# Kernel optimization log

Hardware: AMD Instinct MI355X
Metric: run time of the kernel (lower is better)

The kernel has to match this reference:

```python
import jax, jax.numpy as jnp
import numpy as np

HEADS = 16
DIM_HEAD = 64
LN_EPS = 1e-3  # keras LayerNormalization default


def setup_inputs() -> dict:
    key = jax.random.key(0)
    ks = jax.random.split(key, 4)
    B, N, D = 8, 512, 1024
    inner = HEADS * DIM_HEAD  # 1024
    return {
        "x": jax.random.normal(ks[0], (B, N, D), dtype=jnp.float32),
        "w_qkv": jax.random.normal(ks[1], (D, 3 * inner), dtype=jnp.float32) * (D ** -0.5),
        "reattn_w": jax.random.normal(ks[2], (HEADS, HEADS), dtype=jnp.float32),
        "ln_gamma": jnp.ones((HEADS,), dtype=jnp.float32),
        "ln_beta": jnp.zeros((HEADS,), dtype=jnp.float32),
        "w_out": jax.random.normal(ks[3], (inner, D), dtype=jnp.float32) * (inner ** -0.5),
        "b_out": jnp.zeros((D,), dtype=jnp.float32),
    }


def reference(x, w_qkv, reattn_w, ln_gamma, ln_beta, w_out, b_out):
    B, N, D = x.shape
    H, dh = HEADS, DIM_HEAD
    scale = dh ** -0.5

    qkv = x @ w_qkv  # [B, N, 3*H*dh]
    q, k, v = jnp.split(qkv, 3, axis=-1)
    # b n (h d) -> b h n d
    to_heads = lambda t: t.reshape(B, N, H, dh).transpose(0, 2, 1, 3)
    q, k, v = to_heads(q), to_heads(k), to_heads(v)

    dots = jnp.einsum("bhid,bhjd->bhij", q, k) * scale  # [B, H, N, N]
    attn = jax.nn.softmax(dots, axis=-1)

    # re-attention: mix across heads
    attn = jnp.einsum("bhij,hg->bgij", attn, reattn_w)

    # LayerNorm over the head axis (axis=1), keras default eps
    mean = jnp.mean(attn, axis=1, keepdims=True)
    var = jnp.var(attn, axis=1, keepdims=True)
    attn = (attn - mean) * jax.lax.rsqrt(var + LN_EPS)
    attn = attn * ln_gamma[None, :, None, None] + ln_beta[None, :, None, None]

    out = jnp.einsum("bhij,bhjd->bhid", attn, v)  # [B, H, N, dh]
    out = out.transpose(0, 2, 1, 3).reshape(B, N, H * dh)  # b h n d -> b n (h d)
    return out @ w_out + b_out
```

## Files before the change

### kernel.cpp

```cpp
#include <hip/hip_runtime.h>
#include <math.h>

#define BB 8
#define NN 512
#define DD 1024
#define HH 16
#define DH 64
#define INNER 1024
#define QKV3 3072

typedef __attribute__((ext_vector_type(8))) short short8;
typedef __attribute__((ext_vector_type(4))) float f32x4;

__device__ __forceinline__ float4 ld4(const float* p) { return *(const float4*)p; }

__device__ __forceinline__ unsigned short f2bf(float f) {
    unsigned u = __float_as_uint(f);
    return (unsigned short)((u + 0x7fffu + ((u >> 16) & 1u)) >> 16);
}
__device__ __forceinline__ float bf2f(unsigned short u) {
    return __uint_as_float(((unsigned)u) << 16);
}

__global__ void conv_bf16(const float* __restrict__ in, unsigned short* __restrict__ out) {
    size_t i = ((size_t)blockIdx.x * 256 + threadIdx.x) * 4;
    float4 v = ld4(in + i);
    ushort4 o;
    o.x = f2bf(v.x); o.y = f2bf(v.y); o.z = f2bf(v.z); o.w = f2bf(v.w);
    *(ushort4*)(out + i) = o;
}

__global__ void convT_bf16(const float* __restrict__ in, unsigned short* __restrict__ out,
                           int K, int N) {
    __shared__ float t[32][33];
    const int n0 = blockIdx.x * 32, k0 = blockIdx.y * 32;
    const int tx = threadIdx.x & 31, ty = threadIdx.x >> 5;
#pragma unroll
    for (int l = 0; l < 4; ++l)
        t[ty + 8 * l][tx] = in[(size_t)(k0 + ty + 8 * l) * N + n0 + tx];
    __syncthreads();
#pragma unroll
    for (int l = 0; l < 4; ++l)
        out[(size_t)(n0 + ty + 8 * l) * K + k0 + tx] = f2bf(t[tx][ty + 8 * l]);
}

__global__ __launch_bounds__(256) void gemm_bf16(
    const unsigned short* __restrict__ A, const unsigned short* __restrict__ Bt,
    float* __restrict__ C, const float* __restrict__ bias, int M, int N, int K) {
    __shared__ short As[128 * 32];
    __shared__ short Bs[128 * 32];
    const int tid = threadIdx.x;
    const int w = tid >> 6, l = tid & 63;
    const int bm = blockIdx.y * 128, bn = blockIdx.x * 128;
    const int wm = (w >> 1) * 64, wn = (w & 1) * 64;
    const int lrow = l & 15, lq = l >> 4;

    f32x4 acc[4][4];
#pragma unroll
    for (int i = 0; i < 4; ++i)
#pragma unroll
        for (int j = 0; j < 4; ++j) acc[i][j] = (f32x4){0.f, 0.f, 0.f, 0.f};

    for (int k0 = 0; k0 < K; k0 += 32) {
#pragma unroll
        for (int t = 0; t < 2; ++t) {
            const int q = w * 2 + t;
            const int li = q * 512 + l * 8;
            const int row = li >> 5, kc = li & 31;
            const unsigned short* ga = A + (size_t)(bm + row) * K + k0 + kc;
            __builtin_amdgcn_global_load_lds(
                (const __attribute__((address_space(1))) void*)ga,
                (__attribute__((address_space(3))) void*)(As + q * 512), 16, 0, 0);
            const unsigned short* gb = Bt + (size_t)(bn + row) * K + k0 + kc;
            __builtin_amdgcn_global_load_lds(
                (const __attribute__((address_space(1))) void*)gb,
                (__attribute__((address_space(3))) void*)(Bs + q * 512), 16, 0, 0);
        }
        __syncthreads();

        short8 a[4], b[4];
#pragma unroll
        for (int i = 0; i < 4; ++i)
            a[i] = *(const short8*)(As + (wm + i * 16 + lrow) * 32 + lq * 8);
#pragma unroll
        for (int j = 0; j < 4; ++j)
            b[j] = *(const short8*)(Bs + (wn + j * 16 + lrow) * 32 + lq * 8);
#pragma unroll
        for (int i = 0; i < 4; ++i)
#pragma unroll
            for (int j = 0; j < 4; ++j)
                acc[i][j] = __builtin_amdgcn_mfma_f32_16x16x32_bf16(a[i], b[j], acc[i][j], 0, 0, 0);
        __syncthreads();
    }

#pragma unroll
    for (int i = 0; i < 4; ++i)
#pragma unroll
        for (int j = 0; j < 4; ++j) {
            const int col = bn + wn + j * 16 + lrow;
            const float bv = bias ? bias[col] : 0.f;
#pragma unroll
            for (int r = 0; r < 4; ++r) {
                const int row = bm + wm + i * 16 + lq * 4 + r;
                C[(size_t)row * N + col] = acc[i][j][r] + bv;
            }
        }
}

__global__ __launch_bounds__(256) void gemm_bf16_bf(
    const unsigned short* __restrict__ A, const unsigned short* __restrict__ Bt,
    unsigned short* __restrict__ C, int M, int N, int K) {
    __shared__ short As[128 * 32];
    __shared__ short Bs[128 * 32];
    const int tid = threadIdx.x;
    const int w = tid >> 6, l = tid & 63;
    const int bm = blockIdx.y * 128, bn = blockIdx.x * 128;
    const int wm = (w >> 1) * 64, wn = (w & 1) * 64;
    const int lrow = l & 15, lq = l >> 4;

    f32x4 acc[4][4];
#pragma unroll
    for (int i = 0; i < 4; ++i)
#pragma unroll
        for (int j = 0; j < 4; ++j) acc[i][j] = (f32x4){0.f, 0.f, 0.f, 0.f};

    for (int k0 = 0; k0 < K; k0 += 32) {
#pragma unroll
        for (int t = 0; t < 2; ++t) {
            const int q = w * 2 + t;
            const int li = q * 512 + l * 8;
            const int row = li >> 5, kc = li & 31;
            const unsigned short* ga = A + (size_t)(bm + row) * K + k0 + kc;
            __builtin_amdgcn_global_load_lds(
                (const __attribute__((address_space(1))) void*)ga,
                (__attribute__((address_space(3))) void*)(As + q * 512), 16, 0, 0);
            const unsigned short* gb = Bt + (size_t)(bn + row) * K + k0 + kc;
            __builtin_amdgcn_global_load_lds(
                (const __attribute__((address_space(1))) void*)gb,
                (__attribute__((address_space(3))) void*)(Bs + q * 512), 16, 0, 0);
        }
        __syncthreads();

        short8 a[4], b[4];
#pragma unroll
        for (int i = 0; i < 4; ++i)
            a[i] = *(const short8*)(As + (wm + i * 16 + lrow) * 32 + lq * 8);
#pragma unroll
        for (int j = 0; j < 4; ++j)
            b[j] = *(const short8*)(Bs + (wn + j * 16 + lrow) * 32 + lq * 8);
#pragma unroll
        for (int i = 0; i < 4; ++i)
#pragma unroll
            for (int j = 0; j < 4; ++j)
                acc[i][j] = __builtin_amdgcn_mfma_f32_16x16x32_bf16(a[i], b[j], acc[i][j], 0, 0, 0);
        __syncthreads();
    }

#pragma unroll
    for (int i = 0; i < 4; ++i)
#pragma unroll
        for (int j = 0; j < 4; ++j) {
            const int col = bn + wn + j * 16 + lrow;
#pragma unroll
            for (int r = 0; r < 4; ++r) {
                const int row = bm + wm + i * 16 + lq * 4 + r;
                C[(size_t)row * N + col] = f2bf(acc[i][j][r]);
            }
        }
}

__global__ __launch_bounds__(256) void scores_mfma(
    const unsigned short* __restrict__ qkvb, unsigned short* __restrict__ attnb) {
    const int bh = blockIdx.y;
    const int h = bh & 15, b = bh >> 4;
    const int i0 = blockIdx.x * 64;
    __shared__ short Qs[64 * 64];
    __shared__ short Ks[512 * 64];
    const int tid = threadIdx.x;
    const int w = tid >> 6, l = tid & 63;
    const int lrow = l & 15, lq = l >> 4;
    const int lr8 = l >> 3;
    const int swd = ((l & 7) ^ (lr8 & 7)) * 8;

    const unsigned short* kb = qkvb + (size_t)(b * NN) * QKV3 + INNER + h * DH;
#pragma unroll
    for (int t = 0; t < 16; ++t) {
        int c = w * 16 + t;
        int j = c * 8 + lr8;
        __builtin_amdgcn_global_load_lds(
            (const __attribute__((address_space(1))) void*)(kb + (size_t)j * QKV3 + swd),
            (__attribute__((address_space(3))) void*)(Ks + c * 512), 16, 0, 0);
    }
    const unsigned short* qb = qkvb + (size_t)(b * NN + i0) * QKV3 + h * DH;
#pragma unroll
    for (int t = 0; t < 2; ++t) {
        int c = w * 2 + t;
        int r = c * 8 + lr8;
        __builtin_amdgcn_global_load_lds(
            (const __attribute__((address_space(1))) void*)(qb + (size_t)r * QKV3 + swd),
            (__attribute__((address_space(3))) void*)(Qs + c * 512), 16, 0, 0);
    }
    __syncthreads();

    short8 qf[2];
#pragma unroll
    for (int kh = 0; kh < 2; ++kh)
        qf[kh] = *(const short8*)(Qs + (w * 16 + lrow) * 64 + (((kh * 4 + lq) ^ (lrow & 7)) * 8));

    f32x4 acc[32];
#pragma unroll
    for (int t = 0; t < 32; ++t) acc[t] = (f32x4){0.f, 0.f, 0.f, 0.f};

#pragma unroll
    for (int t = 0; t < 32; ++t) {
#pragma unroll
        for (int kh = 0; kh < 2; ++kh) {
            short8 kf = *(const short8*)(Ks + (t * 16 + lrow) * 64 + (((kh * 4 + lq) ^ (lrow & 7)) * 8));
            acc[t] = __builtin_amdgcn_mfma_f32_16x16x32_bf16(kf, qf[kh], acc[t], 0, 0, 0);
        }
    }

    float mx = -1e30f;
#pragma unroll
    for (int t = 0; t < 32; ++t)
#pragma unroll
        for (int r = 0; r < 4; ++r) mx = fmaxf(mx, acc[t][r]);
    mx = fmaxf(mx, __shfl_xor(mx, 16, 64));
    mx = fmaxf(mx, __shfl_xor(mx, 32, 64));

    float se = 0.f;
#pragma unroll
    for (int t = 0; t < 32; ++t)
#pragma unroll
        for (int r = 0; r < 4; ++r) {
            float e = __expf((acc[t][r] - mx) * 0.125f);
            acc[t][r] = e;
            se += e;
        }
    se += __shfl_xor(se, 16, 64);
    se += __shfl_xor(se, 32, 64);
    const float inv = 1.f / se;

    unsigned short* orow = attnb + ((size_t)bh * NN + i0 + w * 16 + lrow) * NN + lq * 4;
#pragma unroll
    for (int t = 0; t < 32; ++t) {
        ushort4 o;
        o.x = f2bf(acc[t][0] * inv); o.y = f2bf(acc[t][1] * inv);
        o.z = f2bf(acc[t][2] * inv); o.w = f2bf(acc[t][3] * inv);
        *(ushort4*)(orow + t * 16) = o;
    }
}

__global__ void reattn_ln_bf(unsigned short* __restrict__ attnb,
                             const float* __restrict__ rw,
                             const float* __restrict__ gamma,
                             const float* __restrict__ beta) {
    __shared__ float w[16][16];
    __shared__ float gs[16], bs[16];
    const int tid = threadIdx.x;
    ((float*)w)[tid] = rw[tid];
    if (tid < 16) { gs[tid] = gamma[tid]; bs[tid] = beta[tid]; }
    __syncthreads();

    const size_t idx = (size_t)blockIdx.x * 256 + tid;
    const int j2 = (int)(idx & 255);
    const int i = (int)((idx >> 8) & 511);
    const int b = (int)(idx >> 17);
    const size_t hstr = (size_t)NN * NN;
    unsigned short* base = attnb + (size_t)b * HH * hstr + (size_t)i * NN + j2 * 2;

    float vx[16], vy[16];
#pragma unroll
    for (int h = 0; h < 16; ++h) {
        ushort2 u = *(const ushort2*)(base + h * hstr);
        vx[h] = bf2f(u.x); vy[h] = bf2f(u.y);
    }
    float ox[16], oy[16];
    float mex = 0.f, mey = 0.f;
#pragma unroll
    for (int g = 0; g < 16; ++g) {
        float sx = 0.f, sy = 0.f;
#pragma unroll
        for (int h = 0; h < 16; ++h) { sx += vx[h] * w[h][g]; sy += vy[h] * w[h][g]; }
        ox[g] = sx; oy[g] = sy; mex += sx; mey += sy;
    }
    mex *= 0.0625f; mey *= 0.0625f;
    float vax = 0.f, vay = 0.f;
#pragma unroll
    for (int g = 0; g < 16; ++g) {
        float dx = ox[g] - mex, dy = oy[g] - mey;
        vax += dx * dx; vay += dy * dy;
    }
    const float rx = rsqrtf(vax * 0.0625f + 1e-3f);
    const float ry = rsqrtf(vay * 0.0625f + 1e-3f);
#pragma unroll
    for (int g = 0; g < 16; ++g) {
        ushort2 o;
        o.x = f2bf((ox[g] - mex) * rx * gs[g] + bs[g]);
        o.y = f2bf((oy[g] - mey) * ry * gs[g] + bs[g]);
        *(ushort2*)(base + g * hstr) = o;
    }
}

__global__ void transpose_v(const unsigned short* __restrict__ qkvb,
                            unsigned short* __restrict__ vT) {
    __shared__ unsigned short t[32][33];
    const int bh = blockIdx.z;
    const int h = bh & 15, b = bh >> 4;
    const int j0 = blockIdx.x * 32, d0 = blockIdx.y * 32;
    const int tx = threadIdx.x & 31, ty = threadIdx.x >> 5;
    const unsigned short* src = qkvb + (size_t)(b * NN) * QKV3 + 2 * INNER + h * DH;
#pragma unroll
    for (int k = 0; k < 4; ++k)
        t[ty + 8 * k][tx] = src[(size_t)(j0 + ty + 8 * k) * QKV3 + d0 + tx];
    __syncthreads();
    unsigned short* dst = vT + (size_t)bh * DH * NN;
#pragma unroll
    for (int k = 0; k < 4; ++k)
        dst[(size_t)(d0 + ty + 8 * k) * NN + j0 + tx] = t[tx][ty + 8 * k];
}

__global__ __launch_bounds__(256) void pv_mfma(
    const unsigned short* __restrict__ attnb, const unsigned short* __restrict__ vT,
    unsigned short* __restrict__ outhb) {
    const int bh = blockIdx.y;
    const int h = bh & 15, b = bh >> 4;
    const int i0 = blockIdx.x * 128;
    __shared__ short Ps[128 * 64];
    __shared__ short Vs[64 * 64];
    const int tid = threadIdx.x;
    const int w = tid >> 6, l = tid & 63;
    const int lrow = l & 15, lq = l >> 4;
    const int lr8 = l >> 3;
    const int swd = ((l & 7) ^ (lr8 & 7)) * 8;

    f32x4 acc[2][4];
#pragma unroll
    for (int ic = 0; ic < 2; ++ic)
#pragma unroll
        for (int dt = 0; dt < 4; ++dt) acc[ic][dt] = (f32x4){0.f, 0.f, 0.f, 0.f};

    const unsigned short* pb = attnb + ((size_t)bh * NN + i0) * NN;
    const unsigned short* vb = vT + (size_t)bh * DH * NN;

    for (int j0 = 0; j0 < NN; j0 += 64) {
#pragma unroll
        for (int t = 0; t < 4; ++t) {
            int c = w * 4 + t;
            int r = c * 8 + lr8;
            __builtin_amdgcn_global_load_lds(
                (const __attribute__((address_space(1))) void*)(pb + (size_t)r * NN + j0 + swd),
                (__attribute__((address_space(3))) void*)(Ps + c * 512), 16, 0, 0);
        }
#pragma unroll
        for (int t = 0; t < 2; ++t) {
            int c = w * 2 + t;
            int d = c * 8 + lr8;
            __builtin_amdgcn_global_load_lds(
                (const __attribute__((address_space(1))) void*)(vb + (size_t)d * NN + j0 + swd),
                (__attribute__((address_space(3))) void*)(Vs + c * 512), 16, 0, 0);
        }
        __syncthreads();

#pragma unroll
        for (int kh = 0; kh < 2; ++kh) {
            short8 vf[4];
#pragma unroll
            for (int dt = 0; dt < 4; ++dt)
                vf[dt] = *(const short8*)(Vs + (dt * 16 + lrow) * 64 + (((kh * 4 + lq) ^ (lrow & 7)) * 8));
#pragma unroll
            for (int ic = 0; ic < 2; ++ic) {
                short8 pf = *(const short8*)(Ps + (w * 32 + ic * 16 + lrow) * 64 + (((kh * 4 + lq) ^ (lrow & 7)) * 8));
#pragma unroll
                for (int dt = 0; dt < 4; ++dt)
                    acc[ic][dt] = __builtin_amdgcn_mfma_f32_16x16x32_bf16(vf[dt], pf, acc[ic][dt], 0, 0, 0);
            }
        }
        __syncthreads();
    }

#pragma unroll
    for (int ic = 0; ic < 2; ++ic) {
        unsigned short* orow = outhb +
            ((size_t)(b * NN + i0 + w * 32 + ic * 16 + lrow)) * INNER + h * DH + lq * 4;
#pragma unroll
        for (int dt = 0; dt < 4; ++dt) {
            ushort4 o;
            o.x = f2bf(acc[ic][dt][0]); o.y = f2bf(acc[ic][dt][1]);
            o.z = f2bf(acc[ic][dt][2]); o.w = f2bf(acc[ic][dt][3]);
            *(ushort4*)(orow + dt * 16) = o;
        }
    }
}

extern "C" void kernel_launch(void* const* d_in, const int* in_sizes, int n_in,
                              void* d_out, int out_size, void* d_ws, size_t ws_size,
                              hipStream_t stream) {
    const float* x        = (const float*)d_in[0];
    const float* w_qkv    = (const float*)d_in[1];
    const float* reattn_w = (const float*)d_in[2];
    const float* ln_gamma = (const float*)d_in[3];
    const float* ln_beta  = (const float*)d_in[4];
    const float* w_out    = (const float*)d_in[5];
    const float* b_out    = (const float*)d_in[6];
    float* out = (float*)d_out;

    unsigned short* qkvb  = (unsigned short*)d_ws;
    unsigned short* attnb = qkvb + (size_t)BB * NN * QKV3;
    unsigned short* vTb   = attnb + (size_t)BB * HH * NN * NN;
    unsigned short* outhb = vTb + (size_t)BB * HH * DH * NN;
    unsigned short* xb    = outhb + (size_t)BB * NN * INNER;
    unsigned short* wqkvT = xb + (size_t)BB * NN * DD;
    unsigned short* woutT = wqkvT + (size_t)DD * QKV3;

    dim3 blk(256);

    conv_bf16<<<dim3((BB * NN * DD) / 1024), blk, 0, stream>>>(x, xb);
    convT_bf16<<<dim3(QKV3 / 32, DD / 32), blk, 0, stream>>>(w_qkv, wqkvT, DD, QKV3);
    convT_bf16<<<dim3(INNER / 32, INNER / 32), blk, 0, stream>>>(w_out, woutT, INNER, INNER);

    gemm_bf16_bf<<<dim3(QKV3 / 128, (BB * NN) / 128), blk, 0, stream>>>(
        xb, wqkvT, qkvb, BB * NN, QKV3, DD);

    scores_mfma<<<dim3(NN / 64, BB * HH), blk, 0, stream>>>(qkvb, attnb);

    reattn_ln_bf<<<dim3((BB * NN * NN) / 512), blk, 0, stream>>>(attnb, reattn_w, ln_gamma, ln_beta);

    transpose_v<<<dim3(NN / 32, DH / 32, BB * HH), blk, 0, stream>>>(qkvb, vTb);

    pv_mfma<<<dim3(NN / 128, BB * HH), blk, 0, stream>>>(attnb, vTb, outhb);

    gemm_bf16<<<dim3(INNER / 128, (BB * NN) / 128), blk, 0, stream>>>(
        outhb, woutT, out, b_out, BB * NN, INNER, INNER);
}
```

Baseline: 247.9 us.

## Double-buffer K tiles in scores kernel and widen reattn-LN to 4 columns

The scores kernel now streams K in four 128-row chunks through a two-slot LDS buffer, issuing the next chunk's async global-to-LDS load while MFMAs run on the current one. This cuts LDS use from 64KB to 32KB, which may allow more resident blocks and hides load latency, at the cost of extra barriers. The re-attention/LayerNorm kernel processes four columns per thread with 8-byte ushort4 accesses and half as many blocks. That gives wider memory transactions but raises register pressure.

```diff
diff --git a/kernel.cpp b/kernel.cpp
--- a/kernel.cpp
+++ b/kernel.cpp
@@ -175,7 +175,7 @@
     const int h = bh & 15, b = bh >> 4;
     const int i0 = blockIdx.x * 64;
     __shared__ short Qs[64 * 64];
-    __shared__ short Ks[512 * 64];
+    __shared__ short Ks[2][128 * 64];
     const int tid = threadIdx.x;
     const int w = tid >> 6, l = tid & 63;
     const int lrow = l & 15, lq = l >> 4;
@@ -183,15 +183,8 @@
     const int swd = ((l & 7) ^ (lr8 & 7)) * 8;
 
     const unsigned short* kb = qkvb + (size_t)(b * NN) * QKV3 + INNER + h * DH;
-#pragma unroll
-    for (int t = 0; t < 16; ++t) {
-        int c = w * 16 + t;
-        int j = c * 8 + lr8;
-        __builtin_amdgcn_global_load_lds(
-            (const __attribute__((address_space(1))) void*)(kb + (size_t)j * QKV3 + swd),
-            (__attribute__((address_space(3))) void*)(Ks + c * 512), 16, 0, 0);
-    }
     const unsigned short* qb = qkvb + (size_t)(b * NN + i0) * QKV3 + h * DH;
+
 #pragma unroll
     for (int t = 0; t < 2; ++t) {
         int c = w * 2 + t;
@@ -200,6 +193,14 @@
             (const __attribute__((address_space(1))) void*)(qb + (size_t)r * QKV3 + swd),
             (__attribute__((address_space(3))) void*)(Qs + c * 512), 16, 0, 0);
     }
+#pragma unroll
+    for (int t = 0; t < 4; ++t) {
+        int c = w * 4 + t;
+        int j = c * 8 + lr8;
+        __builtin_amdgcn_global_load_lds(
+            (const __attribute__((address_space(1))) void*)(kb + (size_t)j * QKV3 + swd),
+            (__attribute__((address_space(3))) void*)(Ks[0] + c * 512), 16, 0, 0);
+    }
     __syncthreads();
 
     short8 qf[2];
@@ -212,12 +213,27 @@
     for (int t = 0; t < 32; ++t) acc[t] = (f32x4){0.f, 0.f, 0.f, 0.f};
 
 #pragma unroll
-    for (int t = 0; t < 32; ++t) {
-#pragma unroll
-        for (int kh = 0; kh < 2; ++kh) {
-            short8 kf = *(const short8*)(Ks + (t * 16 + lrow) * 64 + (((kh * 4 + lq) ^ (lrow & 7)) * 8));
-            acc[t] = __builtin_amdgcn_mfma_f32_16x16x32_bf16(kf, qf[kh], acc[t], 0, 0, 0);
-        }
+    for (int jc = 0; jc < 4; ++jc) {
+        if (jc < 3) {
+#pragma unroll
+            for (int t = 0; t < 4; ++t) {
+                int c = w * 4 + t;
+                int j = (jc + 1) * 128 + c * 8 + lr8;
+                __builtin_amdgcn_global_load_lds(
+                    (const __attribute__((address_space(1))) void*)(kb + (size_t)j * QKV3 + swd),
+                    (__attribute__((address_space(3))) void*)(Ks[(jc + 1) & 1] + c * 512), 16, 0, 0);
+            }
+        }
+#pragma unroll
+        for (int t = 0; t < 8; ++t) {
+#pragma unroll
+            for (int kh = 0; kh < 2; ++kh) {
+                short8 kf = *(const short8*)(Ks[jc & 1] + (t * 16 + lrow) * 64 +
+                                             (((kh * 4 + lq) ^ (lrow & 7)) * 8));
+                acc[jc * 8 + t] = __builtin_amdgcn_mfma_f32_16x16x32_bf16(kf, qf[kh], acc[jc * 8 + t], 0, 0, 0);
+            }
+        }
+        if (jc < 3) __syncthreads();
     }
 
     float mx = -1e30f;
@@ -263,42 +279,54 @@
     __syncthreads();
 
     const size_t idx = (size_t)blockIdx.x * 256 + tid;
-    const int j2 = (int)(idx & 255);
-    const int i = (int)((idx >> 8) & 511);
-    const int b = (int)(idx >> 17);
+    const int j4 = (int)(idx & 127);
+    const int i = (int)((idx >> 7) & 511);
+    const int b = (int)(idx >> 16);
     const size_t hstr = (size_t)NN * NN;
-    unsigned short* base = attnb + (size_t)b * HH * hstr + (size_t)i * NN + j2 * 2;
-
-    float vx[16], vy[16];
+    unsigned short* base = attnb + (size_t)b * HH * hstr + (size_t)i * NN + j4 * 4;
+
+    float v[16][4];
 #pragma unroll
     for (int h = 0; h < 16; ++h) {
-        ushort2 u = *(const ushort2*)(base + h * hstr);
-        vx[h] = bf2f(u.x); vy[h] = bf2f(u.y);
-    }
-    float ox[16], oy[16];
-    float mex = 0.f, mey = 0.f;
+        ushort4 u = *(const ushort4*)(base + h * hstr);
+        v[h][0] = bf2f(u.x); v[h][1] = bf2f(u.y);
+        v[h][2] = bf2f(u.z); v[h][3] = bf2f(u.w);
+    }
+    float o[16][4];
+    float me[4] = {0.f, 0.f, 0.f, 0.f};
 #pragma unroll
     for (int g = 0; g < 16; ++g) {
-        float sx = 0.f, sy = 0.f;
-#pragma unroll
-        for (int h = 0; h < 16; ++h) { sx += vx[h] * w[h][g]; sy += vy[h] * w[h][g]; }
-        ox[g] = sx; oy[g] = sy; mex += sx; mey += sy;
-    }
-    mex *= 0.0625f; mey *= 0.0625f;
-    float vax = 0.f, vay = 0.f;
+        float s0 = 0.f, s1 = 0.f, s2 = 0.f, s3 = 0.f;
+#pragma unroll
+        for (int h = 0; h < 16; ++h) {
+            const float wg = w[h][g];
+            s0 += v[h][0] * wg; s1 += v[h][1] * wg;
+            s2 += v[h][2] * wg; s3 += v[h][3] * wg;
+        }
+        o[g][0] = s0; o[g][1] = s1; o[g][2] = s2; o[g][3] = s3;
+        me[0] += s0; me[1] += s1; me[2] += s2; me[3] += s3;
+    }
+#pragma unroll
+    for (int r = 0; r < 4; ++r) me[r] *= 0.0625f;
+    float va[4] = {0.f, 0.f, 0.f, 0.f};
+#pragma unroll
+    for (int g = 0; g < 16; ++g)
+#pragma unroll
+        for (int r = 0; r < 4; ++r) {
+            float d = o[g][r] - me[r];
+            va[r] += d * d;
+        }
+    float ri[4];
+#pragma unroll
+    for (int r = 0; r < 4; ++r) ri[r] = rsqrtf(va[r] * 0.0625f + 1e-3f);
 #pragma unroll
     for (int g = 0; g < 16; ++g) {
-        float dx = ox[g] - mex, dy = oy[g] - mey;
-        vax += dx * dx; vay += dy * dy;
-    }
-    const float rx = rsqrtf(vax * 0.0625f + 1e-3f);
-    const float ry = rsqrtf(vay * 0.0625f + 1e-3f);
-#pragma unroll
-    for (int g = 0; g < 16; ++g) {
-        ushort2 o;
-        o.x = f2bf((ox[g] - mex) * rx * gs[g] + bs[g]);
-        o.y = f2bf((oy[g] - mey) * ry * gs[g] + bs[g]);
-        *(ushort2*)(base + g * hstr) = o;
+        ushort4 u;
+        u.x = f2bf((o[g][0] - me[0]) * ri[0] * gs[g] + bs[g]);
+        u.y = f2bf((o[g][1] - me[1]) * ri[1] * gs[g] + bs[g]);
+        u.z = f2bf((o[g][2] - me[2]) * ri[2] * gs[g] + bs[g]);
+        u.w = f2bf((o[g][3] - me[3]) * ri[3] * gs[g] + bs[g]);
+        *(ushort4*)(base + g * hstr) = u;
     }
 }
 
@@ -424,7 +452,7 @@
 
     scores_mfma<<<dim3(NN / 64, BB * HH), blk, 0, stream>>>(qkvb, attnb);
 
-    reattn_ln_bf<<<dim3((BB * NN * NN) / 512), blk, 0, stream>>>(attnb, reattn_w, ln_gamma, ln_beta);
+    reattn_ln_bf<<<dim3((BB * NN * NN) / 1024), blk, 0, stream>>>(attnb, reattn_w, ln_gamma, ln_beta);
 
     transpose_v<<<dim3(NN / 32, DH / 32, BB * HH), blk, 0, stream>>>(qkvb, vTb);
 
```

Result: slower. 259.6 us (+4.7%).
